# Kernel optimization log

Measured on AMD Instinct MI355X. Metric: run time of the kernel, lower is better.

Reference implementation:

```python
import jax, jax.numpy as jnp
import numpy as np

B, T, F, H, S, E, L = 64, 256, 80, 512, 512, 512, 3


def setup_inputs() -> dict:
    key = jax.random.key(0)
    ks = jax.random.split(key, 16)
    sc = 0.05  # keep LSTM gates in a sane range
    inp = {
        "padded_targets": jax.random.normal(ks[0], (B, T, F), jnp.float32),
        "encoder_out": jax.random.normal(ks[1], (B, S, E), jnp.float32),
        "input_seq_lens": jax.random.randint(ks[2], (B,), S // 2, S + 1, jnp.int32),
        "Wih0": jax.random.normal(ks[3], (4 * H, F + E), jnp.float32) * sc,
        "Whh0": jax.random.normal(ks[4], (4 * H, H), jnp.float32) * sc,
        "b0": jax.random.normal(ks[5], (4 * H,), jnp.float32) * sc,
        "Wih1": jax.random.normal(ks[6], (4 * H, H), jnp.float32) * sc,
        "Whh1": jax.random.normal(ks[7], (4 * H, H), jnp.float32) * sc,
        "b1": jax.random.normal(ks[8], (4 * H,), jnp.float32) * sc,
        "Wih2": jax.random.normal(ks[9], (4 * H, H), jnp.float32) * sc,
        "Whh2": jax.random.normal(ks[10], (4 * H, H), jnp.float32) * sc,
        "b2": jax.random.normal(ks[11], (4 * H,), jnp.float32) * sc,
        "Wq": jax.random.normal(ks[12], (H, E), jnp.float32) * sc,
        "Wfc": jax.random.normal(ks[13], (E, F), jnp.float32) * sc,
        "bfc": jax.random.normal(ks[14], (F,), jnp.float32) * sc,
    }
    return inp


def _lstm_cell(x, h, c, Wih, Whh, b):
    g = x @ Wih.T + h @ Whh.T + b                      # [B, 4H]
    i, f, gg, o = jnp.split(g, 4, axis=-1)             # PyTorch gate order i,f,g,o
    c_new = jax.nn.sigmoid(f) * c + jax.nn.sigmoid(i) * jnp.tanh(gg)
    h_new = jax.nn.sigmoid(o) * jnp.tanh(c_new)
    return h_new, c_new


def _decode(padded_targets, encoder_out, mask_bias, params):
    (Wih0, Whh0, b0, Wih1, Whh1, b1, Wih2, Whh2, b2, Wq, Wfc, bfc) = params
    Wihs = (Wih0, Wih1, Wih2)
    Whhs = (Whh0, Whh1, Whh2)
    bs = (b0, b1, b2)
    scale = 1.0 / jnp.sqrt(jnp.asarray(E, jnp.float32))

    def step(carry, xt):
        hs, cs, ctx = carry                            # hs/cs: tuples of [B,H]; ctx [B,E]
        inp = jnp.concatenate([xt, ctx], axis=1)       # [B, F+E]  (teach=1.0 -> always target)
        new_h, new_c = [], []
        for l in range(L):
            hl, cl = _lstm_cell(inp, hs[l], cs[l], Wihs[l], Whhs[l], bs[l])
            new_h.append(hl)
            new_c.append(cl)
            inp = hl
        q = new_h[-1] @ Wq                             # [B,E]
        scores = jnp.einsum('be,bse->bs', q, encoder_out) * scale + mask_bias
        w = jax.nn.softmax(scores, axis=-1)            # [B,S]
        ctx_new = jnp.einsum('bs,bse->be', w, encoder_out)
        pred = ctx_new @ Wfc + bfc                     # [B,F]
        return (tuple(new_h), tuple(new_c), ctx_new), pred

    h0 = tuple(jnp.zeros((B, H), padded_targets.dtype) for _ in range(L))
    c0 = tuple(jnp.zeros((B, H), padded_targets.dtype) for _ in range(L))
    ctx0 = jnp.zeros((B, E), padded_targets.dtype)
    xs = jnp.swapaxes(padded_targets[:, :-1], 0, 1)    # [T-1, B, F]
    _, preds = jax.lax.scan(step, (h0, c0, ctx0), xs)
    return jnp.swapaxes(preds, 0, 1)                   # [B, T-1, F]


def reference(padded_targets, encoder_out, input_seq_lens,
              Wih0, Whh0, b0, Wih1, Whh1, b1, Wih2, Whh2, b2, Wq, Wfc, bfc):
    valid = jnp.arange(S)[None, :] < input_seq_lens[:, None]     # [B,S]
    mask_bias = jnp.where(valid, 0.0, -1e9).astype(jnp.float32)
    params = (Wih0, Whh0, b0, Wih1, Whh1, b1, Wih2, Whh2, b2, Wq, Wfc, bfc)
    return _decode(padded_targets, encoder_out, mask_bias, params)
```

## Files before the change

kernel.cpp:

```cpp
#include <hip/hip_runtime.h>

#define NBLK 256
#define NTHR 512

typedef float f32x4 __attribute__((ext_vector_type(4)));
typedef unsigned int u32;

__device__ __forceinline__ float sigm(float x){ return 1.f/(1.f+__expf(-x)); }
__device__ __forceinline__ float tanh_(float x){ return 1.f - 2.f/(__expf(2.f*x)+1.f); }

__device__ __forceinline__ float wred_sum(float v){
  #pragma unroll
  for (int off=32; off; off>>=1) v += __shfl_xor(v, off, 64);
  return v;
}

__device__ __forceinline__ u32 cvtpk(float lo, float hi){
  u32 r; asm("v_cvt_pk_bf16_f32 %0,%1,%2":"=v"(r):"v"(lo),"v"(hi)); return r;
}
__device__ __forceinline__ float bflo(u32 u){ return __uint_as_float(u<<16); }
__device__ __forceinline__ float bfhi(u32 u){ return __uint_as_float(u & 0xFFFF0000u); }

__device__ __forceinline__ void st_sys(float* p, float v){
  __hip_atomic_store(p, v, __ATOMIC_RELAXED, __HIP_MEMORY_SCOPE_AGENT);
}
__device__ __forceinline__ void st_sysu(u32* p, u32 v){
  __hip_atomic_store(p, v, __ATOMIC_RELAXED, __HIP_MEMORY_SCOPE_AGENT);
}
__device__ __forceinline__ float ald(const float* p){
  return __hip_atomic_load(p, __ATOMIC_RELAXED, __HIP_MEMORY_SCOPE_AGENT);
}
__device__ __forceinline__ u32 aldu(const u32* p){
  return __hip_atomic_load(p, __ATOMIC_RELAXED, __HIP_MEMORY_SCOPE_AGENT);
}

__device__ __forceinline__ void vmwait0(){
  asm volatile("s_waitcnt vmcnt(0)" ::: "memory");
  __builtin_amdgcn_sched_barrier(0);
}
__device__ __forceinline__ void lgkm0(){
  asm volatile("s_waitcnt lgkmcnt(0)" ::: "memory");
  __builtin_amdgcn_sched_barrier(0);
}

__device__ __forceinline__ void gsync(unsigned* bar, int w, unsigned& ep){
  ++ep;
  __builtin_amdgcn_s_waitcnt(0);
  __syncthreads();
  if (threadIdx.x == 0){
    const int g = w >> 4;
    const unsigned epoch = ep;
    bool rootfin = false;
    unsigned o = __hip_atomic_fetch_add(bar + g*32, 1u, __ATOMIC_ACQ_REL, __HIP_MEMORY_SCOPE_AGENT);
    if (o == 15u){
      __hip_atomic_store(bar + g*32, 0u, __ATOMIC_RELAXED, __HIP_MEMORY_SCOPE_AGENT);
      unsigned o2 = __hip_atomic_fetch_add(bar + 16*32, 1u, __ATOMIC_ACQ_REL, __HIP_MEMORY_SCOPE_AGENT);
      if (o2 == 15u){
        __hip_atomic_store(bar + 16*32, 0u, __ATOMIC_RELAXED, __HIP_MEMORY_SCOPE_AGENT);
        __hip_atomic_store(bar + 17*32, epoch, __ATOMIC_RELEASE, __HIP_MEMORY_SCOPE_AGENT);
        rootfin = true;
      }
    }
    if ((w & 15) == 0){
      if (!rootfin){
        while (__hip_atomic_load(bar + 17*32, __ATOMIC_RELAXED, __HIP_MEMORY_SCOPE_AGENT) < epoch)
          __builtin_amdgcn_s_sleep(1);
      }
      __hip_atomic_store(bar + (18+g)*32, epoch, __ATOMIC_RELEASE, __HIP_MEMORY_SCOPE_AGENT);
    } else {
      while (__hip_atomic_load(bar + (18+g)*32, __ATOMIC_RELAXED, __HIP_MEMORY_SCOPE_AGENT) < epoch)
        __builtin_amdgcn_s_sleep(1);
    }
  }
  __syncthreads();
}


template<bool L0T>
__device__ __forceinline__ void lstm_layer(
    int jt, int bt, int tid,
    const float (&wt)[2][8][2], const float (&wx)[2][4],
    float brA, float brB,
    const u32* __restrict__ inu, float* sc_c,
    u32* __restrict__ dstA, int strA,
    u32* __restrict__ dstB, int strB,
    u32* stage, float* scr, u32* xsu, float* sG4,
    const float* __restrict__ tgt, int t)
{
  const int lane = tid & 63, r = tid >> 6;
  const u32* src = inu + bt*16384;

  if (L0T){
    #pragma unroll
    for (int i=0;i<3;++i){
      const int flat = tid + (i<<9);
      if (flat < 1280){
        const int row = flat/40, col = flat - row*40;
        const float* q = tgt + ((((bt<<5)+row)<<8) + t)*80 + (col<<1);
        xsu[flat] = cvtpk(q[0], q[1]);
      }
    }
  }
  uint4 ld[8];
  #pragma unroll
  for (int i=0;i<8;++i){
    const u32* p = src + (i<<11) + (tid<<2);
    asm volatile("global_load_dwordx4 %0, %1, off sc0 sc1" : "=v"(ld[i]) : "v"(p));
  }
  vmwait0();
  #pragma unroll
  for (int i=0;i<8;++i) *(uint4*)(stage + (i<<11) + (tid<<2)) = ld[i];
  __syncthreads();

  float* sw = scr + r*1024;
  #pragma unroll 1
  for (int ch=0; ch<4; ++ch){
    float pv0[8], pv1[8];
    #pragma unroll
    for (int bb=0; bb<8; ++bb){
      const u32* rowp = stage + ((ch<<3)+bb)*512 + lane;
      float a0=0.f,a1=0.f,a2=0.f,a3=0.f, c0=0.f,c1=0.f,c2=0.f,c3=0.f;
      #pragma unroll
      for (int i=0;i<8;i+=2){
        const u32 e0 = rowp[(i<<6)];
        const u32 e1 = rowp[((i+1)<<6)];
        const float f0=bflo(e0), f1=bfhi(e0), f2=bflo(e1), f3=bfhi(e1);
        a0 = fmaf(wt[0][i][0],   f0, a0);
        a1 = fmaf(wt[0][i][1],   f1, a1);
        a2 = fmaf(wt[0][i+1][0], f2, a2);
        a3 = fmaf(wt[0][i+1][1], f3, a3);
        c0 = fmaf(wt[1][i][0],   f0, c0);
        c1 = fmaf(wt[1][i][1],   f1, c1);
        c2 = fmaf(wt[1][i+1][0], f2, c2);
        c3 = fmaf(wt[1][i+1][1], f3, c3);
      }
      if (L0T && lane < 20){
        const int lrow = (ch<<3)+bb;
        const u32 x0 = xsu[lrow*40 + (lane<<1)];
        const u32 x1 = xsu[lrow*40 + (lane<<1) + 1];
        const float g0=bflo(x0), g1=bfhi(x0), g2=bflo(x1), g3=bfhi(x1);
        a0 = fmaf(wx[0][0], g0, a0); a1 = fmaf(wx[0][1], g1, a1);
        a2 = fmaf(wx[0][2], g2, a2); a3 = fmaf(wx[0][3], g3, a3);
        c0 = fmaf(wx[1][0], g0, c0); c1 = fmaf(wx[1][1], g1, c1);
        c2 = fmaf(wx[1][2], g2, c2); c3 = fmaf(wx[1][3], g3, c3);
      }
      pv0[bb] = (a0+a1)+(a2+a3);
      pv1[bb] = (c0+c1)+(c2+c3);
    }
    #pragma unroll
    for (int bb=0; bb<8; ++bb){
      sw[(bb<<6) + lane]       = pv0[bb];
      sw[512 + (bb<<6) + lane] = pv1[bb];
    }
    lgkm0();
    {
      const int bb2 = lane>>3, m = lane&7;
      const float* pp = sw + (bb2<<6) + (m<<3);
      float v0 = ((pp[0]+pp[1])+(pp[2]+pp[3])) + ((pp[4]+pp[5])+(pp[6]+pp[7]));
      const float* pq = pp + 512;
      float v1 = ((pq[0]+pq[1])+(pq[2]+pq[3])) + ((pq[4]+pq[5])+(pq[6]+pq[7]));
      v0 += __shfl_xor(v0,1,64); v0 += __shfl_xor(v0,2,64); v0 += __shfl_xor(v0,4,64);
      v1 += __shfl_xor(v1,1,64); v1 += __shfl_xor(v1,2,64); v1 += __shfl_xor(v1,4,64);
      if (m==0){
        sG4[(((ch<<3)+bb2)<<4) + r]     = v0 + brA;
        sG4[(((ch<<3)+bb2)<<4) + r + 8] = v1 + brB;
      }
    }
  }
  lgkm0();
  __syncthreads();

  if (tid < 128){
    const int b = tid>>2, jl = tid&3;
    const float* g = sG4 + (b<<4) + (jl<<2);
    const float gi = sigm(g[0]), gf = sigm(g[1]);
    const float gg = tanh_(g[2]), go = sigm(g[3]);
    const float cn = gf*sc_c[tid] + gi*gg;
    sc_c[tid] = cn;
    const float hn = go*tanh_(cn);
    const float hn1 = __shfl(hn, tid^1, 64);
    if (!(tid&1)){
      const u32 hp = cvtpk(hn, hn1);
      const int gb = (bt<<5) + b;
      const int col = (jt<<1) + (jl>>1);
      st_sysu(dstA + gb*strA + col, hp);
      st_sysu(dstB + gb*strB + col, hp);
    }
  }
}

#define ZERO_U   212992
#define FP_OFF   212992
#define ENC_OFF  475648
#define ENC_CNT  8388608

__global__ __launch_bounds__(NTHR, 2)
void sd_kernel(const float* __restrict__ tgt,  const float* __restrict__ enc,
               const int*   __restrict__ lens,
               const float* __restrict__ Wih0, const float* __restrict__ Whh0, const float* __restrict__ b0v,
               const float* __restrict__ Wih1, const float* __restrict__ Whh1, const float* __restrict__ b1v,
               const float* __restrict__ Wih2, const float* __restrict__ Whh2, const float* __restrict__ b2v,
               const float* __restrict__ Wq,   const float* __restrict__ Wfc,  const float* __restrict__ bfc,
               float* __restrict__ out, void* __restrict__ wsv, int ebf)
{
  unsigned* bar = (unsigned*)wsv;
  u32* wsu = (u32*)((char*)wsv + 8192);
  u32* IN0u = wsu;
  u32* IN1u = wsu + 65536;
  u32* IN2u = wsu + 131072;
  u32* H2u  = wsu + 196608;
  float* F  = (float*)(wsu + FP_OFF);
  float* QP = F;
  float* PC = F + 131072;
  float* MS = F + 262144;
  u32* encbfu = wsu + ENC_OFF;

  const int w = blockIdx.x, tid = threadIdx.x;
  const int lane = tid & 63, r = tid >> 6;
  const int jt = w >> 1, bt = w & 1;
  unsigned ep = 0;

  __shared__ __attribute__((aligned(16))) u32 SM[26752];
  u32*   stage = SM;
  float* scr   = (float*)(SM + 16384);
  u32*   xsu   = SM + 24576;
  float* sG4   = (float*)(SM + 25856);
  float* sc_c  = (float*)(SM + 26368);
  float* sBig   = (float*)SM;
  float* sVec   = (float*)(SM + 4096);
  float* sSmall = (float*)(SM + 4608);

  const int wrowA = ((r&3)<<9) + (jt<<2) + (r>>2);
  const int wrowB = wrowA + 2;
  float w0r[2][8][2], w1r[2][8][2], w2r[2][8][2], wx0[2][4];
  #pragma unroll
  for (int s=0;s<2;++s){
    const int wr = s ? wrowB : wrowA;
    #pragma unroll
    for (int i=0;i<8;++i){
      const int k = 2*(lane + (i<<6));
      if (k < 512){
        w0r[s][i][0] = Wih0[wr*592 + 80 + k];   w0r[s][i][1] = Wih0[wr*592 + 81 + k];
        w1r[s][i][0] = Wih1[(wr<<9) + k];       w1r[s][i][1] = Wih1[(wr<<9) + k + 1];
        w2r[s][i][0] = Wih2[(wr<<9) + k];       w2r[s][i][1] = Wih2[(wr<<9) + k + 1];
      } else {
        w0r[s][i][0] = Whh0[(wr<<9) + k - 512]; w0r[s][i][1] = Whh0[(wr<<9) + k - 511];
        w1r[s][i][0] = Whh1[(wr<<9) + k - 512]; w1r[s][i][1] = Whh1[(wr<<9) + k - 511];
        w2r[s][i][0] = Whh2[(wr<<9) + k - 512]; w2r[s][i][1] = Whh2[(wr<<9) + k - 511];
      }
    }
    #pragma unroll
    for (int m=0;m<4;++m)
      wx0[s][m] = (lane < 20) ? Wih0[wr*592 + (lane<<2) + m] : 0.f;
  }
  const float br0A=b0v[wrowA], br0B=b0v[wrowB];
  const float br1A=b1v[wrowA], br1B=b1v[wrowB];
  const float br2A=b2v[wrowA], br2B=b2v[wrowB];

  if (tid < 384) sc_c[tid] = 0.f;
  for (int i = w*NTHR + tid; i < ZERO_U; i += NBLK*NTHR) st_sysu(wsu + i, 0u);
  if (ebf){
    for (int i = w*NTHR + tid; i < ENC_CNT; i += NBLK*NTHR)
      st_sysu(encbfu + i, cvtpk(enc[2*i], enc[2*i+1]));
  }
  gsync(bar, w, ep);

  for (int t=0; t<255; ++t){
    const int p = t & 1, np = p ^ 1;
    u32* IN0p = IN0u + p*32768;  u32* IN0n = IN0u + np*32768;
    u32* IN1p = IN1u + p*32768;  u32* IN1n = IN1u + np*32768;
    u32* IN2p = IN2u + p*32768;  u32* IN2n = IN2u + np*32768;

    lstm_layer<true >(jt,bt,tid, w0r, wx0, br0A, br0B, IN0p, sc_c,
                      IN0n+256, 512, IN1p, 512, stage,scr,xsu,sG4, tgt, t);
    gsync(bar,w,ep);
    lstm_layer<false>(jt,bt,tid, w1r, wx0, br1A, br1B, IN1p, sc_c+128,
                      IN1n+256, 512, IN2p, 512, stage,scr,xsu,sG4, tgt, t);
    gsync(bar,w,ep);
    lstm_layer<false>(jt,bt,tid, w2r, wx0, br2A, br2B, IN2p, sc_c+256,
                      IN2n+256, 512, H2u, 256, stage,scr,xsu,sG4, tgt, t);
    gsync(bar,w,ep);

    {
      const int b = w & 63, kq = w >> 6;
      if (tid < 64){
        const u32 u = aldu(H2u + b*256 + kq*64 + tid);
        sVec[2*tid]   = bflo(u);
        sVec[2*tid+1] = bfhi(u);
      }
      __syncthreads();
      const float* wqp = Wq + ((size_t)(kq<<7)<<9) + tid;
      float acc = 0.f;
      #pragma unroll 4
      for (int k=0;k<128;++k) acc = fmaf(sVec[k], wqp[(size_t)k<<9], acc);
      st_sys(&QP[(((kq<<6)+b)<<9) + tid], acc);
    }
    gsync(bar,w,ep);

    {
      const int b = w & 63, sq = w >> 6;
      const int len  = lens[b];
      const int wv = tid >> 6;
      sVec[tid] = ald(&QP[(b<<9)+tid]) + ald(&QP[((64+b)<<9)+tid])
                + ald(&QP[((128+b)<<9)+tid]) + ald(&QP[((192+b)<<9)+tid]);
      __syncthreads();
      const float4 qA = *(const float4*)(sVec + (lane<<3));
      const float4 qB = *(const float4*)(sVec + (lane<<3) + 4);
      float mr = -3.0e38f, lr = 0.f;
      float c0=0,c1=0,c2=0,c3=0,c4=0,c5=0,c6=0,c7=0;
      const float scale = 0.04419417382415922f;
      if (ebf){
        const u32* ebase = encbfu + (((size_t)b)<<17) + (lane<<2);
        #pragma unroll 1
        for (int rr=0; rr<16; ++rr){
          const int srow = (sq<<7) + (wv<<4) + rr;
          if (srow >= len) break;
          const uint4 eu = *(const uint4*)(ebase + ((size_t)srow<<8));
          const float e0=bflo(eu.x), e1=bfhi(eu.x), e2=bflo(eu.y), e3=bfhi(eu.y);
          const float e4=bflo(eu.z), e5=bfhi(eu.z), e6=bflo(eu.w), e7=bfhi(eu.w);
          float d0 = qA.x*e0, d1 = qA.y*e1, d2 = qA.z*e2, d3 = qA.w*e3;
          d0 = fmaf(qB.x, e4, d0); d1 = fmaf(qB.y, e5, d1);
          d2 = fmaf(qB.z, e6, d2); d3 = fmaf(qB.w, e7, d3);
          float d = wred_sum((d0+d1)+(d2+d3));
          const float sc = d*scale;
          const float mn = fmaxf(mr, sc);
          const float sf = __expf(mr - mn);
          const float pe = __expf(sc - mn);
          lr = fmaf(lr, sf, pe);
          c0 = fmaf(c0, sf, pe*e0); c1 = fmaf(c1, sf, pe*e1);
          c2 = fmaf(c2, sf, pe*e2); c3 = fmaf(c3, sf, pe*e3);
          c4 = fmaf(c4, sf, pe*e4); c5 = fmaf(c5, sf, pe*e5);
          c6 = fmaf(c6, sf, pe*e6); c7 = fmaf(c7, sf, pe*e7);
          mr = mn;
        }
      } else {
        #pragma unroll 1
        for (int rr=0; rr<16; ++rr){
          const int srow = (sq<<7) + (wv<<4) + rr;
          if (srow >= len) break;
          const float* ep2 = enc + (((size_t)(b<<9)+srow)<<9) + (lane<<3);
          const float4 e0v = *(const float4*)(ep2);
          const float4 e1v = *(const float4*)(ep2+4);
          float d0 = qA.x*e0v.x, d1 = qA.y*e0v.y, d2 = qA.z*e0v.z, d3 = qA.w*e0v.w;
          d0 = fmaf(qB.x, e1v.x, d0); d1 = fmaf(qB.y, e1v.y, d1);
          d2 = fmaf(qB.z, e1v.z, d2); d3 = fmaf(qB.w, e1v.w, d3);
          float d = wred_sum((d0+d1)+(d2+d3));
          const float sc = d*scale;
          const float mn = fmaxf(mr, sc);
          const float sf = __expf(mr - mn);
          const float pe = __expf(sc - mn);
          lr = fmaf(lr, sf, pe);
          c0 = fmaf(c0, sf, pe*e0v.x); c1 = fmaf(c1, sf, pe*e0v.y);
          c2 = fmaf(c2, sf, pe*e0v.z); c3 = fmaf(c3, sf, pe*e0v.w);
          c4 = fmaf(c4, sf, pe*e1v.x); c5 = fmaf(c5, sf, pe*e1v.y);
          c6 = fmaf(c6, sf, pe*e1v.z); c7 = fmaf(c7, sf, pe*e1v.w);
          mr = mn;
        }
      }
      if (lane==0){ sSmall[wv] = mr; sSmall[8+wv] = lr; }
      {
        float4 v0 = {c0,c1,c2,c3}, v1 = {c4,c5,c6,c7};
        *(float4*)(sBig + (wv<<9) + (lane<<3))     = v0;
        *(float4*)(sBig + (wv<<9) + (lane<<3) + 4) = v1;
      }
      __syncthreads();
      float M = sSmall[0];
      #pragma unroll
      for (int i=1;i<8;++i) M = fmaxf(M, sSmall[i]);
      float L = 0.f, acc = 0.f;
      #pragma unroll
      for (int i=0;i<8;++i){
        const float A = __expf(sSmall[i]-M);
        L   = fmaf(A, sSmall[8+i], L);
        acc = fmaf(A, sBig[(i<<9)+tid], acc);
      }
      st_sys(&PC[(((sq<<6)+b)<<9)+tid], acc);
      if (tid==0){
        st_sys(&MS[(((sq<<6)+b)<<1)],   M);
        st_sys(&MS[(((sq<<6)+b)<<1)+1], L);
      }
    }
    gsync(bar,w,ep);

    if (w < 64){
      const int b = w;
      const float m0 = ald(&MS[(b)<<1]),      S0 = ald(&MS[((b)<<1)+1]);
      const float m1 = ald(&MS[(64+b)<<1]),   S1 = ald(&MS[((64+b)<<1)+1]);
      const float m2 = ald(&MS[(128+b)<<1]),  S2 = ald(&MS[((128+b)<<1)+1]);
      const float m3 = ald(&MS[(192+b)<<1]),  S3 = ald(&MS[((192+b)<<1)+1]);
      const float M  = fmaxf(fmaxf(m0,m1), fmaxf(m2,m3));
      const float a0=__expf(m0-M), a1=__expf(m1-M), a2=__expf(m2-M), a3=__expf(m3-M);
      const float inv = 1.f/(a0*S0 + a1*S1 + a2*S2 + a3*S3);
      const float c = (a0*ald(&PC[(b<<9)+tid])       + a1*ald(&PC[((64+b)<<9)+tid])
                     + a2*ald(&PC[((128+b)<<9)+tid]) + a3*ald(&PC[((192+b)<<9)+tid])) * inv;
      const float c1 = __shfl(c, tid^1, 64);
      if (!(tid&1)) st_sysu(IN0n + b*512 + (tid>>1), cvtpk(c, c1));
      sVec[tid] = c;
      __syncthreads();
      if (tid < 80){
        float acc = 0.f;
        #pragma unroll 4
        for (int e2=0;e2<512;++e2) acc = fmaf(sVec[e2], Wfc[e2*80+tid], acc);
        out[((size_t)b*255 + t)*80 + tid] = acc + bfc[tid];
      }
    }
    gsync(bar,w,ep);
  }
}

extern "C" void kernel_launch(void* const* d_in, const int* in_sizes, int n_in,
                              void* d_out, int out_size, void* d_ws, size_t ws_size,
                              hipStream_t stream) {
  const float* tgt  = (const float*)d_in[0];
  const float* enc  = (const float*)d_in[1];
  const int*   lens = (const int*)  d_in[2];
  const float* Wih0 = (const float*)d_in[3];
  const float* Whh0 = (const float*)d_in[4];
  const float* b0   = (const float*)d_in[5];
  const float* Wih1 = (const float*)d_in[6];
  const float* Whh1 = (const float*)d_in[7];
  const float* b1   = (const float*)d_in[8];
  const float* Wih2 = (const float*)d_in[9];
  const float* Whh2 = (const float*)d_in[10];
  const float* b2   = (const float*)d_in[11];
  const float* Wq   = (const float*)d_in[12];
  const float* Wfc  = (const float*)d_in[13];
  const float* bfc  = (const float*)d_in[14];

  const size_t need = 8192ull + ((size_t)ENC_OFF + (size_t)ENC_CNT)*4ull;
  const int ebf = (ws_size >= need) ? 1 : 0;

  hipMemsetAsync(d_ws, 0, 8192, stream);
  sd_kernel<<<NBLK, NTHR, 0, stream>>>(tgt, enc, lens,
                                       Wih0, Whh0, b0,
                                       Wih1, Whh1, b1,
                                       Wih2, Whh2, b2,
                                       Wq, Wfc, bfc,
                                       (float*)d_out, d_ws, ebf);
}
```

Before: 30.51 ms.

## Merge query, attention and output stages into one per-batch block phase

The query projection, split-S attention and combine stages are collapsed into a single phase run by 64 blocks, one per batch row. This removes two grid-wide barriers per timestep and the global round-trips for partial query, context and softmax statistics. Wq is pre-converted to bf16 in the workspace so each block can compute the full query itself. In exchange, only 64 of 256 blocks do the attention work, with 4x longer serial loops over the sequence per wave, and Wq is now held at reduced precision.

```diff
diff --git a/kernel.cpp b/kernel.cpp
--- a/kernel.cpp
+++ b/kernel.cpp
@@ -21,14 +21,8 @@
 __device__ __forceinline__ float bflo(u32 u){ return __uint_as_float(u<<16); }
 __device__ __forceinline__ float bfhi(u32 u){ return __uint_as_float(u & 0xFFFF0000u); }
 
-__device__ __forceinline__ void st_sys(float* p, float v){
-  __hip_atomic_store(p, v, __ATOMIC_RELAXED, __HIP_MEMORY_SCOPE_AGENT);
-}
 __device__ __forceinline__ void st_sysu(u32* p, u32 v){
   __hip_atomic_store(p, v, __ATOMIC_RELAXED, __HIP_MEMORY_SCOPE_AGENT);
-}
-__device__ __forceinline__ float ald(const float* p){
-  return __hip_atomic_load(p, __ATOMIC_RELAXED, __HIP_MEMORY_SCOPE_AGENT);
 }
 __device__ __forceinline__ u32 aldu(const u32* p){
   return __hip_atomic_load(p, __ATOMIC_RELAXED, __HIP_MEMORY_SCOPE_AGENT);
@@ -74,7 +68,6 @@
   }
   __syncthreads();
 }
-
 
 template<bool L0T>
 __device__ __forceinline__ void lstm_layer(
@@ -190,9 +183,10 @@
 }
 
 #define ZERO_U   212992
-#define FP_OFF   212992
 #define ENC_OFF  475648
 #define ENC_CNT  8388608
+#define WQ_OFF   8864256
+#define WQ_CNT   131072
 
 __global__ __launch_bounds__(NTHR, 2)
 void sd_kernel(const float* __restrict__ tgt,  const float* __restrict__ enc,
@@ -209,11 +203,8 @@
   u32* IN1u = wsu + 65536;
   u32* IN2u = wsu + 131072;
   u32* H2u  = wsu + 196608;
-  float* F  = (float*)(wsu + FP_OFF);
-  float* QP = F;
-  float* PC = F + 131072;
-  float* MS = F + 262144;
   u32* encbfu = wsu + ENC_OFF;
+  u32* wqbfu  = wsu + WQ_OFF;
 
   const int w = blockIdx.x, tid = threadIdx.x;
   const int lane = tid & 63, r = tid >> 6;
@@ -262,6 +253,10 @@
   if (ebf){
     for (int i = w*NTHR + tid; i < ENC_CNT; i += NBLK*NTHR)
       st_sysu(encbfu + i, cvtpk(enc[2*i], enc[2*i+1]));
+    for (int i = w*NTHR + tid; i < WQ_CNT; i += NBLK*NTHR){
+      const int k = i >> 8, ee = (i & 255) << 1;
+      st_sysu(wqbfu + i, cvtpk(Wq[(k<<9) + ee], Wq[(k<<9) + ee + 1]));
+    }
   }
   gsync(bar, w, ep);
 
@@ -281,29 +276,34 @@
                       IN2n+256, 512, H2u, 256, stage,scr,xsu,sG4, tgt, t);
     gsync(bar,w,ep);
 
-    {
-      const int b = w & 63, kq = w >> 6;
-      if (tid < 64){
-        const u32 u = aldu(H2u + b*256 + kq*64 + tid);
+    if (w < 64){
+      const int b = w;
+      const int len = lens[b];
+      if (tid < 256){
+        const u32 u = aldu(H2u + b*256 + tid);
         sVec[2*tid]   = bflo(u);
         sVec[2*tid+1] = bfhi(u);
       }
       __syncthreads();
-      const float* wqp = Wq + ((size_t)(kq<<7)<<9) + tid;
-      float acc = 0.f;
-      #pragma unroll 4
-      for (int k=0;k<128;++k) acc = fmaf(sVec[k], wqp[(size_t)k<<9], acc);
-      st_sys(&QP[(((kq<<6)+b)<<9) + tid], acc);
-    }
-    gsync(bar,w,ep);
-
-    {
-      const int b = w & 63, sq = w >> 6;
-      const int len  = lens[b];
+      float qa = 0.f;
+      if (ebf){
+        const u32* wqb = wqbfu + (tid>>1);
+        const u32 sel = tid & 1;
+        #pragma unroll 4
+        for (int k=0;k<512;++k){
+          const u32 u = wqb[k<<8];
+          qa = fmaf(sVec[k], sel ? bfhi(u) : bflo(u), qa);
+        }
+      } else {
+        const float* wqp = Wq + tid;
+        #pragma unroll 4
+        for (int k=0;k<512;++k) qa = fmaf(sVec[k], wqp[(size_t)k<<9], qa);
+      }
+      __syncthreads();
+      sVec[tid] = qa;
+      __syncthreads();
+
       const int wv = tid >> 6;
-      sVec[tid] = ald(&QP[(b<<9)+tid]) + ald(&QP[((64+b)<<9)+tid])
-                + ald(&QP[((128+b)<<9)+tid]) + ald(&QP[((192+b)<<9)+tid]);
-      __syncthreads();
       const float4 qA = *(const float4*)(sVec + (lane<<3));
       const float4 qB = *(const float4*)(sVec + (lane<<3) + 4);
       float mr = -3.0e38f, lr = 0.f;
@@ -312,8 +312,8 @@
       if (ebf){
         const u32* ebase = encbfu + (((size_t)b)<<17) + (lane<<2);
         #pragma unroll 1
-        for (int rr=0; rr<16; ++rr){
-          const int srow = (sq<<7) + (wv<<4) + rr;
+        for (int rr=0; rr<64; ++rr){
+          const int srow = (wv<<6) + rr;
           if (srow >= len) break;
           const uint4 eu = *(const uint4*)(ebase + ((size_t)srow<<8));
           const float e0=bflo(eu.x), e1=bfhi(eu.x), e2=bflo(eu.y), e3=bfhi(eu.y);
@@ -335,8 +335,8 @@
         }
       } else {
         #pragma unroll 1
-        for (int rr=0; rr<16; ++rr){
-          const int srow = (sq<<7) + (wv<<4) + rr;
+        for (int rr=0; rr<64; ++rr){
+          const int srow = (wv<<6) + rr;
           if (srow >= len) break;
           const float* ep2 = enc + (((size_t)(b<<9)+srow)<<9) + (lane<<3);
           const float4 e0v = *(const float4*)(ep2);
@@ -374,34 +374,16 @@
         L   = fmaf(A, sSmall[8+i], L);
         acc = fmaf(A, sBig[(i<<9)+tid], acc);
       }
-      st_sys(&PC[(((sq<<6)+b)<<9)+tid], acc);
-      if (tid==0){
-        st_sys(&MS[(((sq<<6)+b)<<1)],   M);
-        st_sys(&MS[(((sq<<6)+b)<<1)+1], L);
-      }
-    }
-    gsync(bar,w,ep);
-
-    if (w < 64){
-      const int b = w;
-      const float m0 = ald(&MS[(b)<<1]),      S0 = ald(&MS[((b)<<1)+1]);
-      const float m1 = ald(&MS[(64+b)<<1]),   S1 = ald(&MS[((64+b)<<1)+1]);
-      const float m2 = ald(&MS[(128+b)<<1]),  S2 = ald(&MS[((128+b)<<1)+1]);
-      const float m3 = ald(&MS[(192+b)<<1]),  S3 = ald(&MS[((192+b)<<1)+1]);
-      const float M  = fmaxf(fmaxf(m0,m1), fmaxf(m2,m3));
-      const float a0=__expf(m0-M), a1=__expf(m1-M), a2=__expf(m2-M), a3=__expf(m3-M);
-      const float inv = 1.f/(a0*S0 + a1*S1 + a2*S2 + a3*S3);
-      const float c = (a0*ald(&PC[(b<<9)+tid])       + a1*ald(&PC[((64+b)<<9)+tid])
-                     + a2*ald(&PC[((128+b)<<9)+tid]) + a3*ald(&PC[((192+b)<<9)+tid])) * inv;
-      const float c1 = __shfl(c, tid^1, 64);
-      if (!(tid&1)) st_sysu(IN0n + b*512 + (tid>>1), cvtpk(c, c1));
+      const float c = acc / L;
+      const float cpr = __shfl(c, tid^1, 64);
+      if (!(tid&1)) st_sysu(IN0n + b*512 + (tid>>1), cvtpk(c, cpr));
       sVec[tid] = c;
       __syncthreads();
       if (tid < 80){
-        float acc = 0.f;
+        float acc2 = 0.f;
         #pragma unroll 4
-        for (int e2=0;e2<512;++e2) acc = fmaf(sVec[e2], Wfc[e2*80+tid], acc);
-        out[((size_t)b*255 + t)*80 + tid] = acc + bfc[tid];
+        for (int e2=0;e2<512;++e2) acc2 = fmaf(sVec[e2], Wfc[e2*80+tid], acc2);
+        out[((size_t)b*255 + t)*80 + tid] = acc2 + bfc[tid];
       }
     }
     gsync(bar,w,ep);
@@ -427,7 +409,7 @@
   const float* Wfc  = (const float*)d_in[13];
   const float* bfc  = (const float*)d_in[14];
 
-  const size_t need = 8192ull + ((size_t)ENC_OFF + (size_t)ENC_CNT)*4ull;
+  const size_t need = 8192ull + ((size_t)WQ_OFF + (size_t)WQ_CNT)*4ull;
   const int ebf = (ws_size >= need) ? 1 : 0;
 
   hipMemsetAsync(d_ws, 0, 8192, stream);
```

Result: slower. 37.82 ms (+23.9%).
